# Kernel optimization log

Measured on AMD Instinct MI355X. Metric: run time of the kernel, lower is better.

The kernel has to match this reference:

```python
import jax, jax.numpy as jnp
import numpy as np

# Grid / problem constants
D = H = W_SP = 128      # spatial_shape of the sparse tensor (single batch)
N = 200_000             # number of active voxels
C = 64                  # nchan
K = 5                   # SubMConv3d kernel_size
PAD = 2                 # padding (stride=1 submanifold => output sites == input sites)
EPS = 1e-5              # BatchNorm eps (torch default)


def setup_inputs() -> dict:
    key = jax.random.key(0)
    k1, k2, k3 = jax.random.split(key, 3)
    # unique active voxel coordinates: permute linear grid indices, take first N
    lin = jax.random.permutation(k1, D * H * W_SP)[:N]
    z = lin // (H * W_SP)
    y = (lin // W_SP) % H
    x = lin % W_SP
    coords = jnp.stack([z, y, x], axis=1).astype(jnp.int32)   # [N,3]
    feats = jax.random.normal(k2, (N, C), jnp.float32)        # [N,C]
    std = (2.0 / (K ** 3 * C)) ** 0.5
    Wt = jax.random.normal(k3, (K ** 3, C, C), jnp.float32) * std  # [125,Cin,Cout]
    bias = jnp.full((C,), -0.01, jnp.float32)
    gamma = jnp.ones((C,), jnp.float32)   # bn weight (init 1)
    beta = jnp.zeros((C,), jnp.float32)   # bn bias (init 0)
    return {"feats": feats, "coords": coords, "Wt": Wt, "bias": bias,
            "gamma": gamma, "beta": beta}


def _subm_conv(feats, coords, Wt, bias):
    """Submanifold sparse 3D conv: out[p] = sum_k W_k @ feat[p + off_k], active only."""
    lin = (coords[:, 0] * H + coords[:, 1]) * W_SP + coords[:, 2]
    # dense hash: grid position -> active-voxel row index (or -1)
    idx_map = jnp.full((D * H * W_SP,), -1, jnp.int32).at[lin].set(
        jnp.arange(N, dtype=jnp.int32))
    r = jnp.arange(-PAD, PAD + 1)
    offs = jnp.stack(jnp.meshgrid(r, r, r, indexing="ij"), axis=-1)
    offs = offs.reshape(-1, 3).astype(jnp.int32)              # [125,3]
    bounds = jnp.array([D, H, W_SP], jnp.int32)

    def step(acc, kw):
        Wk, off = kw                                          # [C,C], [3]
        nb = coords + off                                     # [N,3]
        valid = jnp.all((nb >= 0) & (nb < bounds), axis=1)    # [N]
        nlin = (nb[:, 0] * H + nb[:, 1]) * W_SP + nb[:, 2]
        j = idx_map[jnp.where(valid, nlin, 0)]                # [N]
        ok = valid & (j >= 0)
        f = jnp.where(ok[:, None], feats[jnp.maximum(j, 0)], 0.0)  # gather [N,C]
        return acc + f @ Wk, None

    acc0 = jnp.zeros((N, C), feats.dtype)
    out, _ = jax.lax.scan(step, acc0, (Wt, offs))
    return out + bias


def reference(feats, coords, Wt, bias, gamma, beta):
    h = _subm_conv(feats, coords, Wt, bias)
    # BatchNorm1d over active voxels (training-mode batch statistics)
    mean = h.mean(axis=0)
    var = ((h - mean) ** 2).mean(axis=0)
    h = (h - mean) * jax.lax.rsqrt(var + EPS) * gamma + beta
    return jax.nn.elu(h)
```

## Files before the change

### kernel.cpp

```cpp
#include <hip/hip_runtime.h>
#include <hip/hip_bf16.h>

#define NVOX 200000
#define NK   125
#define KCH  25
#define GRID_LIN (128 * 128 * 128)

#define WT_OFF    0u
#define STATS_OFF 1024000u
#define PFX_OFF   1024512u
#define OLD_OFF   1032704u
#define FB_OFF    1832704u
#define IDX_OFF   27432832u

#define F16N   (NVOX * 16)
#define WCONV_N (NK * 4096)
#define PREP_N (F16N + 16 + WCONV_N)

typedef short bf16x8 __attribute__((ext_vector_type(8)));
typedef float f32x4  __attribute__((ext_vector_type(4)));
typedef unsigned short u16x4 __attribute__((ext_vector_type(4)));
typedef unsigned int uint_as1 __attribute__((address_space(1)));
typedef unsigned int uint_as3 __attribute__((address_space(3)));

static __device__ __forceinline__ unsigned short f2bf(float f) {
    union { float f; unsigned int u; } v; v.f = f;
    unsigned int u = v.u;
    return (unsigned short)((u + 0x7FFFu + ((u >> 16) & 1u)) >> 16);
}

__global__ __launch_bounds__(256) void scatter_kernel(const int* __restrict__ coords,
                                                      int* __restrict__ idx_map) {
    int p = blockIdx.x * 256 + threadIdx.x;
    if (p < NVOX) {
        int z = coords[p * 3 + 0], y = coords[p * 3 + 1], x = coords[p * 3 + 2];
        idx_map[(z << 14) | (y << 7) | x] = p;
    }
}

__global__ __launch_bounds__(1024) void count_kernel(const int* __restrict__ idx_map,
                                                     int* __restrict__ pfx) {
    __shared__ int wsum[16];
    int i = blockIdx.x * 1024 + threadIdx.x;
    int bit = idx_map[i] >= 0 ? 1 : 0;
    unsigned long long m = __ballot(bit);
    int lane = threadIdx.x & 63, wave = threadIdx.x >> 6;
    if (lane == 0) wsum[wave] = __popcll(m);
    __syncthreads();
    if (threadIdx.x == 0) {
        int s = 0;
#pragma unroll
        for (int w = 0; w < 16; ++w) s += wsum[w];
        pfx[blockIdx.x] = s;
    }
}

__global__ __launch_bounds__(1024) void scan_kernel(int* __restrict__ pfx) {
    __shared__ int A[2048], B[2048];
    int t = threadIdx.x;
    A[t] = pfx[t]; A[t + 1024] = pfx[t + 1024];
    __syncthreads();
    int* src = A; int* dst = B;
    for (int off = 1; off < 2048; off <<= 1) {
        dst[t]        = src[t]        + (t >= off ? src[t - off] : 0);
        dst[t + 1024] = src[t + 1024] + src[t + 1024 - off];
        __syncthreads();
        int* tmp = src; src = dst; dst = tmp;
    }
    pfx[t]        = t ? src[t - 1] : 0;
    pfx[t + 1024] = src[t + 1023];
}

__global__ __launch_bounds__(1024) void relabel_kernel(const int* __restrict__ pfx,
                                                       int* __restrict__ idx_map,
                                                       int* __restrict__ oldof) {
    __shared__ int wsum[16];
    int i = blockIdx.x * 1024 + threadIdx.x;
    int old = idx_map[i];
    int bit = old >= 0 ? 1 : 0;
    unsigned long long m = __ballot(bit);
    int lane = threadIdx.x & 63, wave = threadIdx.x >> 6;
    int intra = __popcll(m & ((1ull << lane) - 1ull));
    if (lane == 0) wsum[wave] = __popcll(m);
    __syncthreads();
    int woff = 0;
    for (int w = 0; w < wave; ++w) woff += wsum[w];
    if (bit) {
        int nid = pfx[blockIdx.x] + woff + intra;
        idx_map[i] = nid;
        oldof[nid] = old;
    }
}

__global__ __launch_bounds__(256) void prep_kernel(const float* __restrict__ Wt,
                                                   const float* __restrict__ feats,
                                                   const int* __restrict__ oldof,
                                                   unsigned short* __restrict__ wt,
                                                   unsigned short* __restrict__ fb) {
    int i = blockIdx.x * 256 + threadIdx.x;
    if (i < F16N) {
        int p = i >> 4, c = i & 15;
        int old = oldof[p];
        f32x4 f = *(const f32x4*)(feats + (size_t)old * 64 + c * 4);
        u16x4 u;
        u[0] = f2bf(f[0]); u[1] = f2bf(f[1]); u[2] = f2bf(f[2]); u[3] = f2bf(f[3]);
        *(u16x4*)(fb + (size_t)i * 4) = u;
    } else if (i < F16N + 16) {
        *(u16x4*)(fb + (size_t)i * 4) = (u16x4)0;
    } else if (i < PREP_N) {
        int j = i - (F16N + 16);
        int k = j >> 12, r = j & 4095;
        int co = r >> 6, ci = r & 63;
        wt[j] = f2bf(Wt[(k << 12) + (ci << 6) + co]);
    }
}

static __device__ __forceinline__ void stage_w(const unsigned short* wt, int k,
                                               unsigned short* dst, int tid) {
    const unsigned short* src = wt + ((size_t)k << 12) + tid * 8;
    __builtin_amdgcn_global_load_lds((const uint_as1*)(const void*)src,
                                     (uint_as3*)(void*)(dst + tid * 8), 16, 0, 0);
    __builtin_amdgcn_global_load_lds((const uint_as1*)(const void*)(src + 2048),
                                     (uint_as3*)(void*)(dst + tid * 8 + 2048), 16, 0, 0);
}

__global__ __launch_bounds__(256, 2) void conv_kernel(
    const int* __restrict__ coords, const unsigned short* __restrict__ fb,
    const unsigned short* __restrict__ wt, const int* __restrict__ idx_map,
    const int* __restrict__ oldof,
    float* __restrict__ out, float* __restrict__ stats) {
    __shared__ int lds_nbr[KCH * 256];
    __shared__ unsigned short lds_w[2][4096];

    const int vblk = (blockIdx.x & 7) * 98 + (blockIdx.x >> 3);
    const int vbase = vblk * 256;
    if (vbase >= NVOX) return;

    const int tid  = threadIdx.x;
    const int wave = tid >> 6;
    const int lane = tid & 63;
    const int g    = lane >> 4;
    const int l15  = lane & 15;
    const int vox  = vbase + tid;
    const bool live = vox < NVOX;

    int z = 0, y = 0, x = 0;
    if (live) {
        int old = oldof[vox];
        z = coords[old * 3 + 0]; y = coords[old * 3 + 1]; x = coords[old * 3 + 2];
    }
    const int slot = (tid & ~63) | ((tid & 15) << 2) | ((tid >> 4) & 3);

    f32x4 acc[4][4];
#pragma unroll
    for (int a = 0; a < 4; ++a)
#pragma unroll
        for (int b = 0; b < 4; ++b) acc[a][b] = (f32x4)0.0f;

    const char* fbp = (const char*)fb;
    int buf = 0;
    stage_w(wt, 0, &lds_w[0][0], tid);

    for (int c = 0; c < 5; ++c) {
        if (c) __syncthreads();
        const int dz = c - 2, nz = z + dz;
        const bool zok = live && ((unsigned)nz < 128u);
#pragma unroll 5
        for (int kk = 0; kk < KCH; ++kk) {
            int dy = kk / 5 - 2, dx = kk % 5 - 2;
            int ny = y + dy, nx = x + dx;
            int j = NVOX;
            if (zok && ((unsigned)ny < 128u) & ((unsigned)nx < 128u)) {
                int t = idx_map[(nz << 14) | (ny << 7) | nx];
                if (t >= 0) j = t;
            }
            lds_nbr[kk * 256 + slot] = j;
        }
        __syncthreads();

        for (int kk = 0; kk < KCH; ++kk) {
            int k = c * KCH + kk;
            if (k + 1 < NK) stage_w(wt, k + 1, &lds_w[buf ^ 1][0], tid);

            int4 jt4 = *(const int4*)&lds_nbr[kk * 256 + wave * 64 + l15 * 4];
            const int jt[4] = {jt4.x, jt4.y, jt4.z, jt4.w};
            const char* wb = (const char*)&lds_w[buf][0];
#pragma unroll
            for (int s = 0; s < 2; ++s) {
                bf16x8 bfrag[4];
#pragma unroll
                for (int t = 0; t < 4; ++t)
                    bfrag[t] = *(const bf16x8*)(fbp + (((size_t)(unsigned)jt[t] << 7) + (g << 4) + (s << 6)));
#pragma unroll
                for (int a = 0; a < 4; ++a) {
                    bf16x8 afrag = *(const bf16x8*)(wb + (((a * 16 + l15) << 7) + (g << 4) + (s << 6)));
#pragma unroll
                    for (int b = 0; b < 4; ++b)
                        acc[a][b] = __builtin_amdgcn_mfma_f32_16x16x32_bf16(afrag, bfrag[b], acc[a][b], 0, 0, 0);
                }
            }
            buf ^= 1;
            if (kk < KCH - 1) __syncthreads();
        }
    }

#pragma unroll
    for (int b = 0; b < 4; ++b) {
        int v = vbase + wave * 64 + b * 16 + l15;
        if (v < NVOX) {
            int o = oldof[v];
#pragma unroll
            for (int a = 0; a < 4; ++a)
                *(f32x4*)(out + (size_t)o * 64 + a * 16 + g * 4) = acc[a][b];
        }
    }

    float s1[16], s2[16];
#pragma unroll
    for (int a = 0; a < 4; ++a)
#pragma unroll
        for (int r = 0; r < 4; ++r) {
            float s = 0.f, q = 0.f;
#pragma unroll
            for (int b = 0; b < 4; ++b) { float xv = acc[a][b][r]; s += xv; q += xv * xv; }
            s1[a * 4 + r] = s; s2[a * 4 + r] = q;
        }
#pragma unroll
    for (int m = 1; m < 16; m <<= 1) {
#pragma unroll
        for (int i = 0; i < 16; ++i) {
            s1[i] += __shfl_xor(s1[i], m, 64);
            s2[i] += __shfl_xor(s2[i], m, 64);
        }
    }
    if (l15 == 0) {
#pragma unroll
        for (int a = 0; a < 4; ++a)
#pragma unroll
            for (int r = 0; r < 4; ++r) {
                int co = a * 16 + g * 4 + r;
                atomicAdd(&stats[co],      s1[a * 4 + r]);
                atomicAdd(&stats[64 + co], s2[a * 4 + r]);
            }
    }
}

__global__ __launch_bounds__(256) void finalize_kernel(float* __restrict__ out,
                                                       const float* __restrict__ stats,
                                                       const float* __restrict__ gamma,
                                                       const float* __restrict__ beta) {
    int i = blockIdx.x * 256 + threadIdx.x;
    if (i >= NVOX * 16) return;
    int cg = (i & 15) * 4;
    f32x4 v = *(f32x4*)(out + (size_t)i * 4);
    f32x4 r;
#pragma unroll
    for (int c = 0; c < 4; ++c) {
        int co = cg + c;
        float mean = stats[co] * (1.0f / NVOX);
        float var  = stats[64 + co] * (1.0f / NVOX) - mean * mean;
        float sc   = rsqrtf(var + 1e-5f) * gamma[co];
        float sh   = beta[co] - mean * sc;
        float yv   = v[c] * sc + sh;
        r[c] = yv > 0.f ? yv : expm1f(yv);
    }
    *(f32x4*)(out + (size_t)i * 4) = r;
}

extern "C" void kernel_launch(void* const* d_in, const int* in_sizes, int n_in,
                              void* d_out, int out_size, void* d_ws, size_t ws_size,
                              hipStream_t stream) {
    const float* feats  = (const float*)d_in[0];
    const int*   coords = (const int*)d_in[1];
    const float* Wt     = (const float*)d_in[2];
    const float* gamma  = (const float*)d_in[4];
    const float* beta   = (const float*)d_in[5];
    float* out = (float*)d_out;
    char*  ws  = (char*)d_ws;

    unsigned short* wt  = (unsigned short*)(ws + WT_OFF);
    float* stats        = (float*)(ws + STATS_OFF);
    int*   pfx          = (int*)(ws + PFX_OFF);
    int*   oldof        = (int*)(ws + OLD_OFF);
    unsigned short* fb  = (unsigned short*)(ws + FB_OFF);
    int*   idx_map      = (int*)(ws + IDX_OFF);

    hipMemsetAsync(idx_map, 0xFF, (size_t)GRID_LIN * 4, stream);
    hipMemsetAsync(stats, 0, 128 * 4, stream);

    scatter_kernel<<<(NVOX + 255) / 256, 256, 0, stream>>>(coords, idx_map);
    count_kernel<<<GRID_LIN / 1024, 1024, 0, stream>>>(idx_map, pfx);
    scan_kernel<<<1, 1024, 0, stream>>>(pfx);
    relabel_kernel<<<GRID_LIN / 1024, 1024, 0, stream>>>(pfx, idx_map, oldof);
    prep_kernel<<<(PREP_N + 255) / 256, 256, 0, stream>>>(Wt, feats, oldof, wt, fb);
    conv_kernel<<<784, 256, 0, stream>>>(coords, fb, wt, idx_map, oldof, out, stats);
    finalize_kernel<<<12500, 256, 0, stream>>>(out, stats, gamma, beta);
}
```

Baseline: 775.0 us.

## Restructure conv loop into 5-offset groups with swizzled weights and empty-tile skip

Reorganizes the 125-offset loop into 25 groups of 5 x-offsets. Each group stages all 5 weight slices into LDS at once, replacing per-offset double buffering, and needs only one sync pair per group. The weight layout is XOR-swizzled to avoid LDS bank conflicts on A-fragment reads. MFMAs for a 16-voxel column are skipped when no lane in the wave has a valid neighbour. Occupancy hint rises to 3 blocks/SM since the smaller neighbour buffer shrinks LDS use, but weight loads are no longer overlapped with compute.

```diff
diff --git a/kernel.cpp b/kernel.cpp
--- a/kernel.cpp
+++ b/kernel.cpp
@@ -3,7 +3,7 @@
 
 #define NVOX 200000
 #define NK   125
-#define KCH  25
+#define KG   5
 #define GRID_LIN (128 * 128 * 128)
 
 #define WT_OFF    0u
@@ -111,7 +111,8 @@
         int j = i - (F16N + 16);
         int k = j >> 12, r = j & 4095;
         int co = r >> 6, ci = r & 63;
-        wt[j] = f2bf(Wt[(k << 12) + (ci << 6) + co]);
+        int dst = (co << 6) | ((((ci >> 3) ^ (co & 7)) << 3) | (ci & 7));
+        wt[(k << 12) + dst] = f2bf(Wt[(k << 12) + (ci << 6) + co]);
     }
 }
 
@@ -124,13 +125,13 @@
                                      (uint_as3*)(void*)(dst + tid * 8 + 2048), 16, 0, 0);
 }
 
-__global__ __launch_bounds__(256, 2) void conv_kernel(
+__global__ __launch_bounds__(256, 3) void conv_kernel(
     const int* __restrict__ coords, const unsigned short* __restrict__ fb,
     const unsigned short* __restrict__ wt, const int* __restrict__ idx_map,
     const int* __restrict__ oldof,
     float* __restrict__ out, float* __restrict__ stats) {
-    __shared__ int lds_nbr[KCH * 256];
-    __shared__ unsigned short lds_w[2][4096];
+    __shared__ unsigned short lds_w[KG * 4096];
+    __shared__ int lds_nbr[KG * 256];
 
     const int vblk = (blockIdx.x & 7) * 98 + (blockIdx.x >> 3);
     const int vbase = vblk * 256;
@@ -150,6 +151,8 @@
         z = coords[old * 3 + 0]; y = coords[old * 3 + 1]; x = coords[old * 3 + 2];
     }
     const int slot = (tid & ~63) | ((tid & 15) << 2) | ((tid >> 4) & 3);
+    const int sw0 = ((g    ) ^ (l15 & 7)) << 4;
+    const int sw1 = ((g + 4) ^ (l15 & 7)) << 4;
 
     f32x4 acc[4][4];
 #pragma unroll
@@ -158,49 +161,52 @@
         for (int b = 0; b < 4; ++b) acc[a][b] = (f32x4)0.0f;
 
     const char* fbp = (const char*)fb;
-    int buf = 0;
-    stage_w(wt, 0, &lds_w[0][0], tid);
-
-    for (int c = 0; c < 5; ++c) {
-        if (c) __syncthreads();
-        const int dz = c - 2, nz = z + dz;
-        const bool zok = live && ((unsigned)nz < 128u);
-#pragma unroll 5
-        for (int kk = 0; kk < KCH; ++kk) {
-            int dy = kk / 5 - 2, dx = kk % 5 - 2;
-            int ny = y + dy, nx = x + dx;
+
+    for (int grp = 0; grp < NK / KG; ++grp) {
+        __syncthreads();
+#pragma unroll
+        for (int kk = 0; kk < KG; ++kk)
+            stage_w(wt, grp * KG + kk, &lds_w[kk * 4096], tid);
+        const int dz = grp / 5 - 2, dy = grp % 5 - 2;
+        const int nz = z + dz, ny = y + dy;
+        const bool rowok = live && ((unsigned)nz < 128u) && ((unsigned)ny < 128u);
+        const int base = (nz << 14) | (ny << 7);
+#pragma unroll
+        for (int kk = 0; kk < KG; ++kk) {
+            int nx = x + kk - 2;
             int j = NVOX;
-            if (zok && ((unsigned)ny < 128u) & ((unsigned)nx < 128u)) {
-                int t = idx_map[(nz << 14) | (ny << 7) | nx];
+            if (rowok && ((unsigned)nx < 128u)) {
+                int t = idx_map[base | nx];
                 if (t >= 0) j = t;
             }
             lds_nbr[kk * 256 + slot] = j;
         }
         __syncthreads();
 
-        for (int kk = 0; kk < KCH; ++kk) {
-            int k = c * KCH + kk;
-            if (k + 1 < NK) stage_w(wt, k + 1, &lds_w[buf ^ 1][0], tid);
-
+        for (int kk = 0; kk < KG; ++kk) {
             int4 jt4 = *(const int4*)&lds_nbr[kk * 256 + wave * 64 + l15 * 4];
             const int jt[4] = {jt4.x, jt4.y, jt4.z, jt4.w};
-            const char* wb = (const char*)&lds_w[buf][0];
-#pragma unroll
-            for (int s = 0; s < 2; ++s) {
-                bf16x8 bfrag[4];
-#pragma unroll
-                for (int t = 0; t < 4; ++t)
-                    bfrag[t] = *(const bf16x8*)(fbp + (((size_t)(unsigned)jt[t] << 7) + (g << 4) + (s << 6)));
-#pragma unroll
-                for (int a = 0; a < 4; ++a) {
-                    bf16x8 afrag = *(const bf16x8*)(wb + (((a * 16 + l15) << 7) + (g << 4) + (s << 6)));
-#pragma unroll
-                    for (int b = 0; b < 4; ++b)
-                        acc[a][b] = __builtin_amdgcn_mfma_f32_16x16x32_bf16(afrag, bfrag[b], acc[a][b], 0, 0, 0);
+            const char* wb = (const char*)&lds_w[kk * 4096];
+
+            bf16x8 af0[4], af1[4];
+#pragma unroll
+            for (int a = 0; a < 4; ++a) {
+                af0[a] = *(const bf16x8*)(wb + (((a * 16 + l15) << 7) | sw0));
+                af1[a] = *(const bf16x8*)(wb + (((a * 16 + l15) << 7) | sw1));
+            }
+#pragma unroll
+            for (int t = 0; t < 4; ++t) {
+                if (__any(jt[t] != NVOX)) {
+                    const char* rp = fbp + ((size_t)(unsigned)jt[t] << 7) + (g << 4);
+                    bf16x8 b0 = *(const bf16x8*)(rp);
+                    bf16x8 b1 = *(const bf16x8*)(rp + 64);
+#pragma unroll
+                    for (int a = 0; a < 4; ++a) {
+                        acc[a][t] = __builtin_amdgcn_mfma_f32_16x16x32_bf16(af0[a], b0, acc[a][t], 0, 0, 0);
+                        acc[a][t] = __builtin_amdgcn_mfma_f32_16x16x32_bf16(af1[a], b1, acc[a][t], 0, 0, 0);
+                    }
                 }
             }
-            buf ^= 1;
-            if (kk < KCH - 1) __syncthreads();
         }
     }
 
```

Result: faster. 755.7 us (-2.5%).
